# Performance work log

Measured on AMD Instinct MI355X. Metric: run time of the kernel, lower is better.

## Reference

```python
import jax, jax.numpy as jnp
import numpy as np

NH, HD, MBS = 32, 64, 16   # num_heads, head_dim, mini_batch_size
BASE_LR = 1.0
ROPE_BASE = 10000.0
EPS = 1e-6


def _rotate_half(x):
    x1, x2 = jnp.split(x, 2, axis=-1)
    return jnp.concatenate((-x2, x1), axis=-1)


def _permute_qk(x):
    B, H, L, D = x.shape
    return x.reshape(B, H, L, D // 2, 2).swapaxes(-1, -2).reshape(B, H, L, D)


def _undo_permute_qk(x):
    B, H, L, D = x.shape
    return x.reshape(B, H, L, 2, D // 2).swapaxes(-1, -2).reshape(B, H, L, D)


def _ln_fwd(x, gamma, beta):
    mu = x.mean(-1, keepdims=True)
    var = x.var(-1, keepdims=True)
    return gamma * ((x - mu) / jnp.sqrt(var + EPS)) + beta


def _ln_fused_l2_bwd(x, target, gamma, beta):
    # grad of 0.5*||LN(x) - target||^2 wrt x, fused
    D = x.shape[-1]
    mu = x.mean(-1, keepdims=True)
    std = jnp.sqrt(x.var(-1, keepdims=True) + EPS)
    x_hat = (x - mu) / std
    y = gamma * x_hat + beta
    g = (y - target) * gamma
    return (D * g - g.sum(-1, keepdims=True) - x_hat * (g * x_hat).sum(-1, keepdims=True)) / (D * std)


def setup_inputs() -> dict:
    key = jax.random.key(0)
    ks = jax.random.split(key, 8)
    B, L, C, OUT = 4, 2048, 2048, 768
    s = 0.02
    return {
        "hidden_states": jax.random.normal(ks[0], (B, L, C), jnp.float32),
        "position_ids": jnp.broadcast_to(jnp.arange(L, dtype=jnp.int32)[None], (B, L)),
        "Wq": jax.random.normal(ks[1], (C, C), jnp.float32) * s,
        "Wk": jax.random.normal(ks[2], (C, C), jnp.float32) * s,
        "Wv": jax.random.normal(ks[3], (C, C), jnp.float32) * s,
        "Wo": jax.random.normal(ks[4], (C, OUT), jnp.float32) * s,
        "W1": jax.random.normal(ks[5], (NH, HD, HD), jnp.float32) * s,
        "b1": jnp.zeros((NH, 1, HD), jnp.float32),
        "ttt_lr_weight": jax.random.normal(ks[6], (NH, 1, C), jnp.float32) * s,
        "ttt_lr_bias": jnp.zeros((NH, 1), jnp.float32),
        "learnable_token_idx": jnp.zeros((MBS,), jnp.float32),
        "ttt_norm_weight": jnp.ones((NH, HD), jnp.float32),
        "ttt_norm_bias": jnp.zeros((NH, HD), jnp.float32),
        "post_norm_weight": jnp.ones((C,), jnp.float32),
        "post_norm_bias": jnp.zeros((C,), jnp.float32),
    }


def reference(hidden_states, position_ids, Wq, Wk, Wv, Wo, W1, b1,
              ttt_lr_weight, ttt_lr_bias, learnable_token_idx,
              ttt_norm_weight, ttt_norm_bias, post_norm_weight, post_norm_bias):
    B, L, C = hidden_states.shape
    NM = L // MBS
    # QKV projections -> [B, NH, L, HD]
    XQ = (hidden_states @ Wq).reshape(B, L, NH, HD).transpose(0, 2, 1, 3)
    XK = (hidden_states @ Wk).reshape(B, L, NH, HD).transpose(0, 2, 1, 3)
    XV = (hidden_states @ Wv).reshape(B, L, NH, HD).transpose(0, 2, 1, 3)
    # RoPE on positions modulo the mini-batch size
    pos = (position_ids % MBS).astype(jnp.float32)  # [B, L]
    inv_freq = 1.0 / (ROPE_BASE ** (jnp.arange(0, HD, 2, dtype=jnp.float32) / HD))
    freqs = pos[..., None] * inv_freq               # [B, L, HD/2]
    emb = jnp.concatenate((freqs, freqs), axis=-1)  # [B, L, HD]
    cos = jnp.cos(emb)[:, None]                     # [B, 1, L, HD]
    sin = jnp.sin(emb)[:, None]
    XQ, XK = _permute_qk(XQ), _permute_qk(XK)
    XQ = XQ * cos + _rotate_half(XQ) * sin
    XK = XK * cos + _rotate_half(XK) * sin
    XQ, XK = _undo_permute_qk(XQ), _undo_permute_qk(XK)
    # reshape into mini-batches: [B, NH, NM, K, HD]
    X = hidden_states.reshape(B, NM, MBS, C)
    XQ = XQ.reshape(B, NH, NM, MBS, HD)
    XK = XK.reshape(B, NH, NM, MBS, HD)
    XV = XV.reshape(B, NH, NM, MBS, HD)
    # eta: per-token learnable LR gate
    ttt_lr = jax.nn.sigmoid(
        jnp.einsum('bnkc,hdc->bhnkd', X, ttt_lr_weight)
        + ttt_lr_bias.reshape(1, NH, 1, 1, 1))              # [B,NH,NM,K,1]
    ttt_lr_eta = BASE_LR * ttt_lr.transpose(0, 1, 2, 4, 3) / HD  # [B,NH,NM,1,K]
    token_idx = jnp.clip(1.0 / jnp.arange(1, MBS + 1, dtype=jnp.float32)
                         + learnable_token_idx, 0.0, None)
    token_eta = token_idx.reshape(1, 1, 1, MBS, 1)
    eta = token_eta * ttt_lr_eta                            # [B,NH,NM,K,K]
    # TTT-Linear dual-form mini-batch scan
    ln_w = ttt_norm_weight.reshape(1, NH, 1, HD)
    ln_b = ttt_norm_bias.reshape(1, NH, 1, HD)
    W1_0 = jnp.broadcast_to(W1[None], (B, NH, HD, HD))
    b1_0 = jnp.broadcast_to(b1[None], (B, NH, 1, HD))
    tril = jnp.tril(jnp.ones((MBS, MBS), hidden_states.dtype))

    def step(carry, xs):
        W1_s, b1_s = carry
        xq, xk, xv, eta_m = xs                 # [B,NH,K,HD], eta_m [B,NH,K,K]
        Z1 = xk @ W1_s + b1_s
        target = xv - xk
        grad = _ln_fused_l2_bwd(Z1, target, ln_w, ln_b)
        Attn = tril * (xq @ xk.swapaxes(-1, -2))
        b1_bar = b1_s - (tril * eta_m) @ grad
        Z1_bar = xq @ W1_s - (eta_m * Attn) @ grad + b1_bar
        last_eta = eta_m[:, :, -1, :, None]    # [B,NH,K,1]
        W1_new = W1_s - (last_eta * xk).swapaxes(-1, -2) @ grad
        b1_new = b1_s - jnp.sum(last_eta * grad, axis=-2, keepdims=True)
        out = xq + _ln_fwd(Z1_bar, ln_w, ln_b)
        return (W1_new, b1_new), out

    xs = (XQ.transpose(2, 0, 1, 3, 4), XK.transpose(2, 0, 1, 3, 4),
          XV.transpose(2, 0, 1, 3, 4), eta.transpose(2, 0, 1, 3, 4))
    _, outs = jax.lax.scan(step, (W1_0, b1_0), xs)   # [NM,B,NH,K,HD]
    out = outs.transpose(1, 2, 0, 3, 4).reshape(B, NH, L, HD)
    out = out.transpose(0, 2, 1, 3).reshape(B, L, C)
    # post LayerNorm (eps 1e-6) and output projection
    mu = out.mean(-1, keepdims=True)
    var = out.var(-1, keepdims=True)
    out = (out - mu) / jnp.sqrt(var + EPS) * post_norm_weight + post_norm_bias
    return out @ Wo
```

## Files before the change

kernel.cpp:

```cpp
#include <hip/hip_runtime.h>
#include <cstddef>
#include <cstdint>

#define B_DIM   4
#define L_SEQ   2048
#define C_DIM   2048
#define OUT_DIM 768
#define NHEADS  32
#define HDIM    64
#define MBS_    16
#define NMINI   128
#define EPS_    1e-6f

typedef _Float16 half8 __attribute__((ext_vector_type(8)));
typedef float floatx4 __attribute__((ext_vector_type(4)));

__device__ __forceinline__ void glds16(const void* g, void* l) {
    __builtin_amdgcn_global_load_lds(
        (const __attribute__((address_space(1))) uint32_t*)g,
        (__attribute__((address_space(3))) uint32_t*)l, 16, 0, 0);
}

__device__ __forceinline__ void split8(const float4 a, const float4 b,
                                       half8& hi, half8& lo) {
    const float x[8] = {a.x, a.y, a.z, a.w, b.x, b.y, b.z, b.w};
#pragma unroll
    for (int e = 0; e < 8; e++) {
        const _Float16 h = (_Float16)x[e];
        hi[e] = h;
        lo[e] = (_Float16)(x[e] - (float)h);
    }
}

#define MFMA3(ACC, AH, AL, BH, BL)                                             \
    ACC = __builtin_amdgcn_mfma_f32_16x16x32_f16((AH), (BH), ACC, 0, 0, 0);    \
    ACC = __builtin_amdgcn_mfma_f32_16x16x32_f16((AH), (BL), ACC, 0, 0, 0);    \
    ACC = __builtin_amdgcn_mfma_f32_16x16x32_f16((AL), (BH), ACC, 0, 0, 0);

#define BARRIER_LGKM() __asm volatile("s_waitcnt lgkmcnt(0)\n\ts_barrier" ::: "memory")
#define WAIT_VM0()     __asm volatile("s_waitcnt vmcnt(0)" ::: "memory")

__global__ __launch_bounds__(256)
void gemm_af32(const float* __restrict__ A,
               const _Float16* __restrict__ Bhi, const _Float16* __restrict__ Blo,
               float* __restrict__ Cout, int mode, int doRope)
{
    __shared__ __align__(16) float    sA[4096];
    __shared__ __align__(16) _Float16 sBhi[4096];
    __shared__ __align__(16) _Float16 sBlo[4096];
    const int tid = threadIdx.x;
    const int m0 = blockIdx.y * 128, n0 = blockIdx.x * 128;
    const int K = 2048;

    size_t gA[4]; float* lA[4];
#pragma unroll
    for (int I = 0; I < 4; I++) {
        const int c = I * 256 + tid;
        const int row = c >> 3, seg = (c & 7) ^ (row & 7);
        gA[I] = (size_t)(m0 + row) * K + seg * 4;
        lA[I] = &sA[c * 4];
    }
    size_t gB[2]; _Float16 *lBh[2], *lBl[2];
#pragma unroll
    for (int I = 0; I < 2; I++) {
        const int c = I * 256 + tid;
        const int row = c >> 2, seg = (c & 3) ^ ((row >> 1) & 3);
        gB[I] = (size_t)(n0 + row) * K + seg * 8;
        lBh[I] = &sBhi[c * 8];
        lBl[I] = &sBlo[c * 8];
    }

    const int lane = tid & 63, quad = lane >> 4, lc = lane & 15;
    const int wv = tid >> 6, wm = wv & 1, wn = wv >> 1;
    int offA0[4], offA1[4], offB[4];
#pragma unroll
    for (int i = 0; i < 4; i++) {
        const int rA = wm * 64 + i * 16 + lc;
        offA0[i] = (rA * 8 + ((2 * quad)     ^ (rA & 7))) * 4;
        offA1[i] = (rA * 8 + ((2 * quad + 1) ^ (rA & 7))) * 4;
    }
#pragma unroll
    for (int j = 0; j < 4; j++) {
        const int rB = wn * 64 + j * 16 + lc;
        offB[j] = (rB * 4 + (quad ^ ((rB >> 1) & 3))) * 8;
    }

    floatx4 acc[4][4];
#pragma unroll
    for (int i = 0; i < 4; i++)
#pragma unroll
        for (int j = 0; j < 4; j++) acc[i][j] = (floatx4)0.0f;

    for (int k0 = 0; k0 < K; k0 += 32) {
        __syncthreads();
#pragma unroll
        for (int I = 0; I < 4; I++) glds16(A + gA[I] + k0, lA[I]);
#pragma unroll
        for (int I = 0; I < 2; I++) {
            glds16(Bhi + gB[I] + k0, lBh[I]);
            glds16(Blo + gB[I] + k0, lBl[I]);
        }
        __syncthreads();

        half8 ah[4], al[4], bh[4], bl[4];
#pragma unroll
        for (int i = 0; i < 4; i++) {
            const float4 va = *(const float4*)&sA[offA0[i]];
            const float4 vb = *(const float4*)&sA[offA1[i]];
            split8(va, vb, ah[i], al[i]);
        }
#pragma unroll
        for (int j = 0; j < 4; j++) {
            bh[j] = *(const half8*)&sBhi[offB[j]];
            bl[j] = *(const half8*)&sBlo[offB[j]];
        }
#pragma unroll
        for (int i = 0; i < 4; i++)
#pragma unroll
            for (int j = 0; j < 4; j++) {
                MFMA3(acc[i][j], ah[i], al[i], bh[j], bl[j]);
            }
    }

    float cs[4][4], sn[4][4];
    if (doRope) {
#pragma unroll
        for (int j = 0; j < 4; j++) {
            const int ii = ((j * 16 + lc) & 63) >> 1;
            const float invf = expf(-(float)ii * 0.28782313662425574f);
#pragma unroll
            for (int r = 0; r < 4; r++) {
                const float ang = (float)(quad * 4 + r) * invf;
                sincosf(ang, &sn[j][r], &cs[j][r]);
            }
        }
    }
    const int oddcol = lc & 1;
#pragma unroll
    for (int i = 0; i < 4; i++) {
#pragma unroll
        for (int j = 0; j < 4; j++) {
            floatx4 v = acc[i][j];
            if (doRope) {
#pragma unroll
                for (int r = 0; r < 4; r++) {
                    const float partner = __shfl_xor(v[r], 1);
                    v[r] = v[r] * cs[j][r] + partner * (oddcol ? sn[j][r] : -sn[j][r]);
                }
            }
            const int n = n0 + wn * 64 + j * 16 + lc;
            if (mode == 0) {
                const int h = (n >> 6) & 31, d = n & 63;
#pragma unroll
                for (int r = 0; r < 4; r++) {
                    const int m = m0 + wm * 64 + i * 16 + quad * 4 + r;
                    const int b = m >> 11, li = m & 2047;
                    Cout[((size_t)(b * 32 + h) * 2048 + li) * 64 + d] = v[r];
                }
            } else {
#pragma unroll
                for (int r = 0; r < 4; r++) {
                    const int m = m0 + wm * 64 + i * 16 + quad * 4 + r;
                    Cout[(size_t)m * OUT_DIM + n] = v[r];
                }
            }
        }
    }
}

__global__ __launch_bounds__(256)
void wtrans_kernel(const float* __restrict__ W, _Float16* __restrict__ BThi,
                   _Float16* __restrict__ BTlo, int Nw)
{
    __shared__ float tile[32][33];
    const int t = threadIdx.x, tx = t & 31, ty = t >> 5;
    const int n0 = blockIdx.x * 32, k0 = blockIdx.y * 32;
    const int K = 2048;
#pragma unroll
    for (int r = 0; r < 4; r++)
        tile[ty + r * 8][tx] = W[(size_t)(k0 + ty + r * 8) * Nw + n0 + tx];
    __syncthreads();
#pragma unroll
    for (int r = 0; r < 4; r++) {
        const float val = tile[tx][ty + r * 8];
        const _Float16 hh = (_Float16)val;
        const size_t o = (size_t)(n0 + ty + r * 8) * K + k0 + tx;
        BThi[o] = hh;
        BTlo[o] = (_Float16)(val - (float)hh);
    }
}

__global__ __launch_bounds__(256)
void lr_kernel(const float* __restrict__ hidden, const float* __restrict__ wlr,
               const float* __restrict__ lr_bias, float* __restrict__ lrs)
{
    __shared__ float sRow[2048];
    __shared__ float sPart[32][9];
    const int m = blockIdx.x;
    const int t = threadIdx.x;
    const float* row = hidden + (size_t)m * C_DIM;
#pragma unroll
    for (int j = 0; j < 8; j++) sRow[t + j * 256] = row[t + j * 256];
    __syncthreads();
    const int h = t >> 3, p = t & 7;
    const float* w = wlr + (size_t)h * C_DIM;
    float s = 0.0f;
#pragma unroll 8
    for (int k = 0; k < 64; k++) {
        const int c = k * 32 + p * 4;
        const float4 a = *(const float4*)(sRow + c);
        const float4 b = *(const float4*)(w + c);
        s += a.x * b.x + a.y * b.y + a.z * b.z + a.w * b.w;
    }
    sPart[h][p] = s;
    __syncthreads();
    if (t < 32) {
        float v = 0.0f;
#pragma unroll
        for (int p2 = 0; p2 < 8; p2++) v += sPart[t][p2];
        v += lr_bias[t];
        const float sig = 1.0f / (1.0f + expf(-v));
        lrs[((size_t)(m >> 11) * NHEADS + t) * L_SEQ + (m & 2047)] = sig;
    }
}

__global__ __launch_bounds__(256, 1)
void scan_v6(const float* __restrict__ XQ, const float* __restrict__ XK,
             float* __restrict__ XVo, const float* __restrict__ LRS,
             const float* __restrict__ W1i, const float* __restrict__ b1i,
             const float* __restrict__ lt, const float* __restrict__ lnw,
             const float* __restrict__ lnb)
{
    __shared__ __align__(16) float sXq[2][1024];
    __shared__ __align__(16) float sXk[2][1024];
    __shared__ __align__(16) float sXv[2][1024];
    __shared__ __align__(16) float sW1T[4096];
    __shared__ __align__(16) float sGt[64 * 36];
    __shared__ __align__(16) float sKt[64 * 36];
    __shared__ __align__(16) float sCf[16 * 36];
    __shared__ __align__(16) float sRedA[16 * 8];
    __shared__ __align__(16) float sRedB[16 * 8];
    __shared__ __align__(16) float sRedC[16 * 8];
    __shared__ __align__(16) float sB1[64];
    __shared__ __align__(16) float sEta[32];

    const int t = threadIdx.x;
    const int lane = t & 63, q = lane >> 4, lc = lane & 15;
    const int w = t >> 6;
    const int col = 16 * w + lc;
    const int bh = blockIdx.x, h = bh & 31;

    int srcOffW;
    {
        const int c = w * 64 + lane;
        const int row = c >> 4, seg = (c & 15) ^ (row & 15);
        srcOffW = row * 64 + seg * 4;
    }

    float tokR[4];
#pragma unroll
    for (int r = 0; r < 4; r++)
        tokR[r] = fmaxf(1.0f / (float)(4 * q + r + 1) + lt[4 * q + r], 0.0f);
    const float tok15 = fmaxf(1.0f / 16.0f + lt[15], 0.0f);
    const float gamC = lnw[h * 64 + col], betC = lnb[h * 64 + col];

    if (t < 64) sB1[t] = b1i[h * 64 + t];
    if (t < 32) sEta[t] = 0.0f;
    for (int z = t; z < 1024; z += 256) {
        const int r = z >> 4, c = 16 + (z & 15);
        sGt[r * 36 + c] = 0.0f;
        sKt[r * 36 + c] = 0.0f;
    }
    { const int r = t >> 4, c = 16 + (t & 15); sCf[r * 36 + c] = 0.0f; }

    float w1s[4][4];
#pragma unroll
    for (int t4 = 0; t4 < 4; t4++)
#pragma unroll
        for (int r = 0; r < 4; r++)
            w1s[t4][r] = W1i[h * 4096 + (16 * t4 + lc) * 64 + (16 * w + 4 * q + r)];
#pragma unroll
    for (int t4 = 0; t4 < 4; t4++)
#pragma unroll
        for (int r = 0; r < 4; r++) {
            const int nn = 16 * w + 4 * q + r, k = 16 * t4 + lc;
            sW1T[nn * 64 + ((((k >> 2) ^ (nn & 15)) << 2) | (k & 3))] = w1s[t4][r];
        }

    const size_t base = (size_t)bh * L_SEQ * HDIM;
    const float* xq_g = XQ + base;
    const float* xk_g = XK + base;
    float* xv_g = XVo + base;
    const float* lr_g = LRS + (size_t)bh * L_SEQ;

    glds16(xq_g + srcOffW, &sXq[0][w * 256]);
    glds16(xk_g + srcOffW, &sXk[0][w * 256]);
    glds16(xv_g + srcOffW, &sXv[0][w * 256]);
    float clr = lr_g[lc];

    for (int n = 0; n < NMINI; n++) {
        const int buf = n & 1, nb = buf ^ 1;
        WAIT_VM0();
        BARRIER_LGKM();

        const float etaC = clr * (1.0f / 64.0f);
        if (w == 0 && t < 16) sEta[t] = etaC;
        const int np = (n + 1) & (NMINI - 1);
        const size_t go = (size_t)np * 1024;
        glds16(xq_g + go + srcOffW, &sXq[nb][w * 256]);
        glds16(xk_g + go + srcOffW, &sXk[nb][w * 256]);
        glds16(xv_g + go + srcOffW, &sXv[nb][w * 256]);
        const float nlr = lr_g[np * 16 + lc];

        const float b1c = sB1[col];

        {
            const int phys = q + 4 * w;
            const float4 v = *(const float4*)&sXk[buf][lc * 64 + phys * 4];
            const int cb = 4 * (phys ^ lc);
            const float leC = tok15 * etaC;
            sKt[(cb + 0) * 36 + lc] = v.x * leC;
            sKt[(cb + 1) * 36 + lc] = v.y * leC;
            sKt[(cb + 2) * 36 + lc] = v.z * leC;
            sKt[(cb + 3) * 36 + lc] = v.w * leC;
        }

        half8 qh[2], ql[2], kh[2], kl[2], wh[2], wl[2];
#pragma unroll
        for (int f = 0; f < 2; f++) {
            const int ca = (8 * f + 2 * q) ^ lc, cb2 = (8 * f + 2 * q + 1) ^ lc;
            {
                const float4 u0 = *(const float4*)&sXq[buf][lc * 64 + ca * 4];
                const float4 u1 = *(const float4*)&sXq[buf][lc * 64 + cb2 * 4];
                split8(u0, u1, qh[f], ql[f]);
            }
            {
                const float4 u0 = *(const float4*)&sXk[buf][lc * 64 + ca * 4];
                const float4 u1 = *(const float4*)&sXk[buf][lc * 64 + cb2 * 4];
                split8(u0, u1, kh[f], kl[f]);
            }
            {
                const int rw = 16 * w + lc;
                const float4 u0 = *(const float4*)&sW1T[rw * 64 + ca * 4];
                const float4 u1 = *(const float4*)&sW1T[rw * 64 + cb2 * 4];
                split8(u0, u1, wh[f], wl[f]);
            }
        }

        floatx4 at = (floatx4)0.0f, z1a = (floatx4)0.0f, zba = (floatx4)0.0f;
        if (w == 0) {
#pragma unroll
            for (int f = 0; f < 2; f++) { MFMA3(at, qh[f], ql[f], kh[f], kl[f]); }
        }
#pragma unroll
        for (int f = 0; f < 2; f++) {
            MFMA3(z1a, kh[f], kl[f], wh[f], wl[f]);
            MFMA3(zba, qh[f], ql[f], wh[f], wl[f]);
        }

        float z[4], s1[4], s2[4];
#pragma unroll
        for (int r = 0; r < 4; r++) { z[r] = z1a[r] + b1c; s1[r] = z[r]; s2[r] = z[r] * z[r]; }
#pragma unroll
        for (int o = 1; o < 16; o <<= 1)
#pragma unroll
            for (int r = 0; r < 4; r++) { s1[r] += __shfl_xor(s1[r], o); s2[r] += __shfl_xor(s2[r], o); }
        if (lc == 0)
#pragma unroll
            for (int r = 0; r < 4; r++) {
                sRedA[(4 * q + r) * 8 + w] = s1[r];
                sRedA[(4 * q + r) * 8 + 4 + w] = s2[r];
            }
        BARRIER_LGKM();
        float mu[4], rs[4];
#pragma unroll
        for (int r = 0; r < 4; r++) {
            const float4 a = *(const float4*)&sRedA[(4 * q + r) * 8];
            const float4 b = *(const float4*)&sRedA[(4 * q + r) * 8 + 4];
            const float m1 = (a.x + a.y + a.z + a.w) * (1.0f / 64.0f);
            mu[r] = m1;
            rs[r] = rsqrtf((b.x + b.y + b.z + b.w) * (1.0f / 64.0f) - m1 * m1 + EPS_);
        }

        float gg[4], xh[4], g1[4], g2[4];
#pragma unroll
        for (int r = 0; r < 4; r++) {
            const int row = 4 * q + r;
            const int ad = row * 64 + (((((col >> 2) ^ row) & 15) << 2) | (col & 3));
            xh[r] = (z[r] - mu[r]) * rs[r];
            const float tgt = sXv[buf][ad] - sXk[buf][ad];
            gg[r] = (gamC * xh[r] + betC - tgt) * gamC;
            g1[r] = gg[r];
            g2[r] = gg[r] * xh[r];
        }
#pragma unroll
        for (int o = 1; o < 16; o <<= 1)
#pragma unroll
            for (int r = 0; r < 4; r++) { g1[r] += __shfl_xor(g1[r], o); g2[r] += __shfl_xor(g2[r], o); }
        if (lc == 0)
#pragma unroll
            for (int r = 0; r < 4; r++) {
                sRedB[(4 * q + r) * 8 + w] = g1[r];
                sRedB[(4 * q + r) * 8 + 4 + w] = g2[r];
            }
        BARRIER_LGKM();
        {
            float4 g4;
#pragma unroll
            for (int r = 0; r < 4; r++) {
                const float4 a = *(const float4*)&sRedB[(4 * q + r) * 8];
                const float4 b = *(const float4*)&sRedB[(4 * q + r) * 8 + 4];
                const float G1 = a.x + a.y + a.z + a.w;
                const float G2 = b.x + b.y + b.z + b.w;
                ((float*)&g4)[r] = (64.0f * gg[r] - G1 - xh[r] * G2) * rs[r] * (1.0f / 64.0f);
            }
            *(float4*)&sGt[col * 36 + 4 * q] = g4;
        }
        if (w == 0) {
#pragma unroll
            for (int r = 0; r < 4; r++) {
                const int i = 4 * q + r;
                sCf[i * 36 + lc] = (lc <= i) ? -tokR[r] * etaC * (at[r] + 1.0f) : 0.0f;
            }
        }
        BARRIER_LGKM();

        half8 cfh, cfl, gth, gtl;
        {
            const float4 u0 = *(const float4*)&sCf[lc * 36 + 8 * q];
            const float4 u1 = *(const float4*)&sCf[lc * 36 + 8 * q + 4];
            split8(u0, u1, cfh, cfl);
        }
        {
            const int rw = 16 * w + lc;
            const float4 u0 = *(const float4*)&sGt[rw * 36 + 8 * q];
            const float4 u1 = *(const float4*)&sGt[rw * 36 + 8 * q + 4];
            split8(u0, u1, gth, gtl);
        }
        MFMA3(zba, cfh, cfl, gth, gtl);
#pragma unroll
        for (int t4 = 0; t4 < 4; t4++) {
            half8 kth, ktl;
            const float4 u0 = *(const float4*)&sKt[(16 * t4 + lc) * 36 + 8 * q];
            const float4 u1 = *(const float4*)&sKt[(16 * t4 + lc) * 36 + 8 * q + 4];
            split8(u0, u1, kth, ktl);
            floatx4 up = (floatx4)0.0f;
            MFMA3(up, gth, gtl, kth, ktl);
#pragma unroll
            for (int r = 0; r < 4; r++) w1s[t4][r] -= up[r];
        }

        float z2[4];
#pragma unroll
        for (int r = 0; r < 4; r++) { z2[r] = zba[r] + b1c; s1[r] = z2[r]; s2[r] = z2[r] * z2[r]; }
#pragma unroll
        for (int o = 1; o < 16; o <<= 1)
#pragma unroll
            for (int r = 0; r < 4; r++) { s1[r] += __shfl_xor(s1[r], o); s2[r] += __shfl_xor(s2[r], o); }
        if (lc == 0)
#pragma unroll
            for (int r = 0; r < 4; r++) {
                sRedC[(4 * q + r) * 8 + w] = s1[r];
                sRedC[(4 * q + r) * 8 + 4 + w] = s2[r];
            }
        BARRIER_LGKM();
#pragma unroll
        for (int r = 0; r < 4; r++) {
            const float4 a = *(const float4*)&sRedC[(4 * q + r) * 8];
            const float4 b = *(const float4*)&sRedC[(4 * q + r) * 8 + 4];
            const float m1 = (a.x + a.y + a.z + a.w) * (1.0f / 64.0f);
            mu[r] = m1;
            rs[r] = rsqrtf((b.x + b.y + b.z + b.w) * (1.0f / 64.0f) - m1 * m1 + EPS_);
        }
#pragma unroll
        for (int r = 0; r < 4; r++) {
            const int row = 4 * q + r;
            const int ad = row * 64 + (((((col >> 2) ^ row) & 15) << 2) | (col & 3));
            xv_g[n * 1024 + row * 64 + col] =
                sXq[buf][ad] + gamC * ((z2[r] - mu[r]) * rs[r]) + betC;
        }

        {
            const float4 e0 = *(const float4*)&sEta[8 * q];
            const float4 e1 = *(const float4*)&sEta[8 * q + 4];
            const float ev[8] = {e0.x, e0.y, e0.z, e0.w, e1.x, e1.y, e1.z, e1.w};
            float p = 0.0f;
#pragma unroll
            for (int jj = 0; jj < 8; jj++)
                p += ((float)gth[jj] + (float)gtl[jj]) * ev[jj];
            p += __shfl_xor(p, 16);
            if (q == 0) sB1[col] -= tok15 * p;
        }

#pragma unroll
        for (int t4 = 0; t4 < 4; t4++)
#pragma unroll
            for (int r = 0; r < 4; r++) {
                const int nn = 16 * w + 4 * q + r, k = 16 * t4 + lc;
                sW1T[nn * 64 + ((((k >> 2) ^ (nn & 15)) << 2) | (k & 3))] = w1s[t4][r];
            }
        clr = nlr;
    }
}

__global__ __launch_bounds__(256)
void postln_kernel(const float* __restrict__ Ob, const float* __restrict__ pnw,
                   const float* __restrict__ pnb, float* __restrict__ XN)
{
    const int m = blockIdx.x;
    const int b = m >> 11, l = m & 2047;
    const int t = threadIdx.x;
    float v[8];
    float s1 = 0.0f, s2 = 0.0f;
    const float* bas = Ob + (size_t)b * NHEADS * L_SEQ * HDIM + (size_t)l * HDIM;
#pragma unroll
    for (int j = 0; j < 8; j++) {
        const int c = t + j * 256;
        const int hh = c >> 6, d = c & 63;
        const float x = bas[(size_t)hh * (L_SEQ * HDIM) + d];
        v[j] = x; s1 += x; s2 += x * x;
    }
#pragma unroll
    for (int o = 1; o < 64; o <<= 1) { s1 += __shfl_xor(s1, o); s2 += __shfl_xor(s2, o); }
    __shared__ float r1[4], r2[4];
    const int w = t >> 6;
    if ((t & 63) == 0) { r1[w] = s1; r2[w] = s2; }
    __syncthreads();
    s1 = r1[0] + r1[1] + r1[2] + r1[3];
    s2 = r2[0] + r2[1] + r2[2] + r2[3];
    const float mu = s1 * (1.0f / 2048.0f);
    const float var = s2 * (1.0f / 2048.0f) - mu * mu;
    const float rstd = rsqrtf(var + EPS_);
    float* o = XN + (size_t)m * C_DIM;
#pragma unroll
    for (int j = 0; j < 8; j++) {
        const int c = t + j * 256;
        o[c] = (v[j] - mu) * rstd * pnw[c] + pnb[c];
    }
}

extern "C" void kernel_launch(void* const* d_in, const int* in_sizes, int n_in,
                              void* d_out, int out_size, void* d_ws, size_t ws_size,
                              hipStream_t stream)
{
    (void)in_sizes; (void)n_in; (void)out_size; (void)ws_size;
    const float* hidden  = (const float*)d_in[0];
    const float* Wq      = (const float*)d_in[2];
    const float* Wk      = (const float*)d_in[3];
    const float* Wv      = (const float*)d_in[4];
    const float* Wo      = (const float*)d_in[5];
    const float* W1      = (const float*)d_in[6];
    const float* b1      = (const float*)d_in[7];
    const float* wlr     = (const float*)d_in[8];
    const float* lr_bias = (const float*)d_in[9];
    const float* lt      = (const float*)d_in[10];
    const float* lnw     = (const float*)d_in[11];
    const float* lnb     = (const float*)d_in[12];
    const float* pnw     = (const float*)d_in[13];
    const float* pnb     = (const float*)d_in[14];

    const size_t TEN = (size_t)B_DIM * NHEADS * L_SEQ * HDIM;
    float* XQ  = (float*)d_ws;
    float* XK  = XQ + TEN;
    float* XVo = XK + TEN;
    float* LRS = XVo + TEN;
    const dim3 blk(256);

    _Float16* BThi = (_Float16*)d_out;
    _Float16* BTlo = BThi + (size_t)C_DIM * C_DIM;

    lr_kernel<<<dim3(B_DIM * L_SEQ), blk, 0, stream>>>(hidden, wlr, lr_bias, LRS);

    const float* Wmats[3] = {Wq, Wk, Wv};
    float* outs[3] = {XQ, XK, XVo};
    for (int p = 0; p < 3; p++) {
        wtrans_kernel<<<dim3(64, 64), blk, 0, stream>>>(Wmats[p], BThi, BTlo, C_DIM);
        gemm_af32<<<dim3(16, 64), blk, 0, stream>>>(hidden, BThi, BTlo,
                                                    outs[p], 0, (p < 2) ? 1 : 0);
    }
    scan_v6<<<dim3(B_DIM * NHEADS), blk, 0, stream>>>(XQ, XK, XVo, LRS,
                                                      W1, b1, lt, lnw, lnb);
    float* XN = XQ;
    _Float16* WThi = (_Float16*)XK;
    _Float16* WTlo = WThi + (size_t)OUT_DIM * C_DIM;
    postln_kernel<<<dim3(B_DIM * L_SEQ), blk, 0, stream>>>(XVo, pnw, pnb, XN);
    wtrans_kernel<<<dim3(24, 64), blk, 0, stream>>>(Wo, WThi, WTlo, OUT_DIM);
    gemm_af32<<<dim3(6, 64), blk, 0, stream>>>(XN, WThi, WTlo,
                                               (float*)d_out, 1, 0);
}
```

Before: 1.611 ms.

## Restructure TTT scan to cut barriers and pass gradients via shuffles

Result: faster. 1.512 ms (-6.1%).

```diff
diff --git a/kernel.cpp b/kernel.cpp
--- a/kernel.cpp
+++ b/kernel.cpp
@@ -32,13 +32,19 @@
     }
 }
 
+__device__ __forceinline__ void split8f(const float x[8], half8& hi, half8& lo) {
+#pragma unroll
+    for (int e = 0; e < 8; e++) {
+        const _Float16 h = (_Float16)x[e];
+        hi[e] = h;
+        lo[e] = (_Float16)(x[e] - (float)h);
+    }
+}
+
 #define MFMA3(ACC, AH, AL, BH, BL)                                             \
     ACC = __builtin_amdgcn_mfma_f32_16x16x32_f16((AH), (BH), ACC, 0, 0, 0);    \
     ACC = __builtin_amdgcn_mfma_f32_16x16x32_f16((AH), (BL), ACC, 0, 0, 0);    \
     ACC = __builtin_amdgcn_mfma_f32_16x16x32_f16((AL), (BH), ACC, 0, 0, 0);
-
-#define BARRIER_LGKM() __asm volatile("s_waitcnt lgkmcnt(0)\n\ts_barrier" ::: "memory")
-#define WAIT_VM0()     __asm volatile("s_waitcnt vmcnt(0)" ::: "memory")
 
 __global__ __launch_bounds__(256)
 void gemm_af32(const float* __restrict__ A,
@@ -225,7 +231,7 @@
 }
 
 __global__ __launch_bounds__(256, 1)
-void scan_v6(const float* __restrict__ XQ, const float* __restrict__ XK,
+void scan_v8(const float* __restrict__ XQ, const float* __restrict__ XK,
              float* __restrict__ XVo, const float* __restrict__ LRS,
              const float* __restrict__ W1i, const float* __restrict__ b1i,
              const float* __restrict__ lt, const float* __restrict__ lnw,
@@ -235,14 +241,12 @@
     __shared__ __align__(16) float sXk[2][1024];
     __shared__ __align__(16) float sXv[2][1024];
     __shared__ __align__(16) float sW1T[4096];
-    __shared__ __align__(16) float sGt[64 * 36];
     __shared__ __align__(16) float sKt[64 * 36];
     __shared__ __align__(16) float sCf[16 * 36];
-    __shared__ __align__(16) float sRedA[16 * 8];
-    __shared__ __align__(16) float sRedB[16 * 8];
-    __shared__ __align__(16) float sRedC[16 * 8];
+    __shared__ __align__(16) float sRedA[128];
+    __shared__ __align__(16) float sRedB[128];
+    __shared__ __align__(16) float sRedC[128];
     __shared__ __align__(16) float sB1[64];
-    __shared__ __align__(16) float sEta[32];
 
     const int t = threadIdx.x;
     const int lane = t & 63, q = lane >> 4, lc = lane & 15;
@@ -250,11 +254,12 @@
     const int col = 16 * w + lc;
     const int bh = blockIdx.x, h = bh & 31;
 
-    int srcOffW;
+    int srcOffW, ldsOff;
     {
         const int c = w * 64 + lane;
         const int row = c >> 4, seg = (c & 15) ^ (row & 15);
         srcOffW = row * 64 + seg * 4;
+        ldsOff = c * 4;
     }
 
     float tokR[4];
@@ -265,10 +270,8 @@
     const float gamC = lnw[h * 64 + col], betC = lnb[h * 64 + col];
 
     if (t < 64) sB1[t] = b1i[h * 64 + t];
-    if (t < 32) sEta[t] = 0.0f;
     for (int z = t; z < 1024; z += 256) {
         const int r = z >> 4, c = 16 + (z & 15);
-        sGt[r * 36 + c] = 0.0f;
         sKt[r * 36 + c] = 0.0f;
     }
     { const int r = t >> 4, c = 16 + (t & 15); sCf[r * 36 + c] = 0.0f; }
@@ -293,26 +296,44 @@
     float* xv_g = XVo + base;
     const float* lr_g = LRS + (size_t)bh * L_SEQ;
 
-    glds16(xq_g + srcOffW, &sXq[0][w * 256]);
-    glds16(xk_g + srcOffW, &sXk[0][w * 256]);
-    glds16(xv_g + srcOffW, &sXv[0][w * 256]);
+    {
+        const float4 q0 = *(const float4*)(xq_g + srcOffW);
+        const float4 k0 = *(const float4*)(xk_g + srcOffW);
+        const float4 v0 = *(const float4*)(xv_g + srcOffW);
+        *(float4*)&sXq[0][ldsOff] = q0;
+        *(float4*)&sXk[0][ldsOff] = k0;
+        *(float4*)&sXv[0][ldsOff] = v0;
+    }
     float clr = lr_g[lc];
+    __syncthreads();
+
+    int adR[4];
+#pragma unroll
+    for (int r = 0; r < 4; r++) {
+        const int row = 4 * q + r;
+        adR[r] = row * 64 + (((((col >> 2) ^ row) & 15) << 2) | (col & 3));
+    }
 
     for (int n = 0; n < NMINI; n++) {
         const int buf = n & 1, nb = buf ^ 1;
-        WAIT_VM0();
-        BARRIER_LGKM();
-
-        const float etaC = clr * (1.0f / 64.0f);
-        if (w == 0 && t < 16) sEta[t] = etaC;
+
         const int np = (n + 1) & (NMINI - 1);
         const size_t go = (size_t)np * 1024;
-        glds16(xq_g + go + srcOffW, &sXq[nb][w * 256]);
-        glds16(xk_g + go + srcOffW, &sXk[nb][w * 256]);
-        glds16(xv_g + go + srcOffW, &sXv[nb][w * 256]);
+        const float4 nq = *(const float4*)(xq_g + go + srcOffW);
+        const float4 nk = *(const float4*)(xk_g + go + srcOffW);
+        const float4 nv = *(const float4*)(xv_g + go + srcOffW);
         const float nlr = lr_g[np * 16 + lc];
 
+        const float etaC = clr * (1.0f / 64.0f);
         const float b1c = sB1[col];
+
+        float xvR[4], xkR[4], xqR[4];
+#pragma unroll
+        for (int r = 0; r < 4; r++) {
+            xvR[r] = sXv[buf][adR[r]];
+            xkR[r] = sXk[buf][adR[r]];
+            xqR[r] = sXq[buf][adR[r]];
+        }
 
         {
             const int phys = q + 4 * w;
@@ -358,6 +379,14 @@
             MFMA3(zba, qh[f], ql[f], wh[f], wl[f]);
         }
 
+        if (w == 0) {
+#pragma unroll
+            for (int r = 0; r < 4; r++) {
+                const int i = 4 * q + r;
+                sCf[i * 36 + lc] = (lc <= i) ? -tokR[r] * etaC * (at[r] + 1.0f) : 0.0f;
+            }
+        }
+
         float z[4], s1[4], s2[4];
 #pragma unroll
         for (int r = 0; r < 4; r++) { z[r] = z1a[r] + b1c; s1[r] = z[r]; s2[r] = z[r] * z[r]; }
@@ -371,7 +400,8 @@
                 sRedA[(4 * q + r) * 8 + w] = s1[r];
                 sRedA[(4 * q + r) * 8 + 4 + w] = s2[r];
             }
-        BARRIER_LGKM();
+        __syncthreads();
+
         float mu[4], rs[4];
 #pragma unroll
         for (int r = 0; r < 4; r++) {
@@ -385,10 +415,8 @@
         float gg[4], xh[4], g1[4], g2[4];
 #pragma unroll
         for (int r = 0; r < 4; r++) {
-            const int row = 4 * q + r;
-            const int ad = row * 64 + (((((col >> 2) ^ row) & 15) << 2) | (col & 3));
             xh[r] = (z[r] - mu[r]) * rs[r];
-            const float tgt = sXv[buf][ad] - sXk[buf][ad];
+            const float tgt = xvR[r] - xkR[r];
             gg[r] = (gamC * xh[r] + betC - tgt) * gamC;
             g1[r] = gg[r];
             g2[r] = gg[r] * xh[r];
@@ -403,41 +431,34 @@
                 sRedB[(4 * q + r) * 8 + w] = g1[r];
                 sRedB[(4 * q + r) * 8 + 4 + w] = g2[r];
             }
-        BARRIER_LGKM();
+        __syncthreads();
+
+        float gradReg[4];
+#pragma unroll
+        for (int r = 0; r < 4; r++) {
+            const float4 a = *(const float4*)&sRedB[(4 * q + r) * 8];
+            const float4 b = *(const float4*)&sRedB[(4 * q + r) * 8 + 4];
+            const float G1 = a.x + a.y + a.z + a.w;
+            const float G2 = b.x + b.y + b.z + b.w;
+            gradReg[r] = (64.0f * gg[r] - G1 - xh[r] * G2) * rs[r] * (1.0f / 64.0f);
+        }
+        half8 gth, gtl;
         {
-            float4 g4;
-#pragma unroll
-            for (int r = 0; r < 4; r++) {
-                const float4 a = *(const float4*)&sRedB[(4 * q + r) * 8];
-                const float4 b = *(const float4*)&sRedB[(4 * q + r) * 8 + 4];
-                const float G1 = a.x + a.y + a.z + a.w;
-                const float G2 = b.x + b.y + b.z + b.w;
-                ((float*)&g4)[r] = (64.0f * gg[r] - G1 - xh[r] * G2) * rs[r] * (1.0f / 64.0f);
-            }
-            *(float4*)&sGt[col * 36 + 4 * q] = g4;
-        }
-        if (w == 0) {
-#pragma unroll
-            for (int r = 0; r < 4; r++) {
-                const int i = 4 * q + r;
-                sCf[i * 36 + lc] = (lc <= i) ? -tokR[r] * etaC * (at[r] + 1.0f) : 0.0f;
-            }
-        }
-        BARRIER_LGKM();
-
-        half8 cfh, cfl, gth, gtl;
+            float gv[8];
+#pragma unroll
+            for (int jj = 0; jj < 8; jj++) {
+                const float v = __shfl(gradReg[jj & 3], ((q * 8 + jj) >> 2) * 16 + lc);
+                gv[jj] = (q < 2) ? v : 0.0f;
+            }
+            split8f(gv, gth, gtl);
+        }
         {
+            half8 cfh, cfl;
             const float4 u0 = *(const float4*)&sCf[lc * 36 + 8 * q];
             const float4 u1 = *(const float4*)&sCf[lc * 36 + 8 * q + 4];
             split8(u0, u1, cfh, cfl);
-        }
-        {
-            const int rw = 16 * w + lc;
-            const float4 u0 = *(const float4*)&sGt[rw * 36 + 8 * q];
-            const float4 u1 = *(const float4*)&sGt[rw * 36 + 8 * q + 4];
-            split8(u0, u1, gth, gtl);
-        }
-        MFMA3(zba, cfh, cfl, gth, gtl);
+            MFMA3(zba, cfh, cfl, gth, gtl);
+        }
 #pragma unroll
         for (int t4 = 0; t4 < 4; t4++) {
             half8 kth, ktl;
@@ -449,7 +470,25 @@
 #pragma unroll
             for (int r = 0; r < 4; r++) w1s[t4][r] -= up[r];
         }
-
+        {
+            float p = 0.0f;
+#pragma unroll
+            for (int r = 0; r < 4; r++)
+                p += __shfl(etaC, 4 * q + r) * gradReg[r];
+            p += __shfl_xor(p, 16);
+            p += __shfl_xor(p, 32);
+            if (q == 0) sB1[col] -= tok15 * p;
+        }
+        *(float4*)&sXq[nb][ldsOff] = nq;
+        *(float4*)&sXk[nb][ldsOff] = nk;
+        *(float4*)&sXv[nb][ldsOff] = nv;
+#pragma unroll
+        for (int t4 = 0; t4 < 4; t4++)
+#pragma unroll
+            for (int r = 0; r < 4; r++) {
+                const int nn = 16 * w + 4 * q + r, k = 16 * t4 + lc;
+                sW1T[nn * 64 + ((((k >> 2) ^ (nn & 15)) << 2) | (k & 3))] = w1s[t4][r];
+            }
         float z2[4];
 #pragma unroll
         for (int r = 0; r < 4; r++) { z2[r] = zba[r] + b1c; s1[r] = z2[r]; s2[r] = z2[r] * z2[r]; }
@@ -463,42 +502,18 @@
                 sRedC[(4 * q + r) * 8 + w] = s1[r];
                 sRedC[(4 * q + r) * 8 + 4 + w] = s2[r];
             }
-        BARRIER_LGKM();
+        __syncthreads();
+
 #pragma unroll
         for (int r = 0; r < 4; r++) {
             const float4 a = *(const float4*)&sRedC[(4 * q + r) * 8];
             const float4 b = *(const float4*)&sRedC[(4 * q + r) * 8 + 4];
             const float m1 = (a.x + a.y + a.z + a.w) * (1.0f / 64.0f);
-            mu[r] = m1;
-            rs[r] = rsqrtf((b.x + b.y + b.z + b.w) * (1.0f / 64.0f) - m1 * m1 + EPS_);
-        }
-#pragma unroll
-        for (int r = 0; r < 4; r++) {
+            const float rr = rsqrtf((b.x + b.y + b.z + b.w) * (1.0f / 64.0f) - m1 * m1 + EPS_);
             const int row = 4 * q + r;
-            const int ad = row * 64 + (((((col >> 2) ^ row) & 15) << 2) | (col & 3));
             xv_g[n * 1024 + row * 64 + col] =
-                sXq[buf][ad] + gamC * ((z2[r] - mu[r]) * rs[r]) + betC;
-        }
-
-        {
-            const float4 e0 = *(const float4*)&sEta[8 * q];
-            const float4 e1 = *(const float4*)&sEta[8 * q + 4];
-            const float ev[8] = {e0.x, e0.y, e0.z, e0.w, e1.x, e1.y, e1.z, e1.w};
-            float p = 0.0f;
-#pragma unroll
-            for (int jj = 0; jj < 8; jj++)
-                p += ((float)gth[jj] + (float)gtl[jj]) * ev[jj];
-            p += __shfl_xor(p, 16);
-            if (q == 0) sB1[col] -= tok15 * p;
-        }
-
-#pragma unroll
-        for (int t4 = 0; t4 < 4; t4++)
-#pragma unroll
-            for (int r = 0; r < 4; r++) {
-                const int nn = 16 * w + 4 * q + r, k = 16 * t4 + lc;
-                sW1T[nn * 64 + ((((k >> 2) ^ (nn & 15)) << 2) | (k & 3))] = w1s[t4][r];
-            }
+                xqR[r] + gamC * ((z2[r] - m1) * rr) + betC;
+        }
         clr = nlr;
     }
 }
@@ -578,7 +593,7 @@
         gemm_af32<<<dim3(16, 64), blk, 0, stream>>>(hidden, BThi, BTlo,
                                                     outs[p], 0, (p < 2) ? 1 : 0);
     }
-    scan_v6<<<dim3(B_DIM * NHEADS), blk, 0, stream>>>(XQ, XK, XVo, LRS,
+    scan_v8<<<dim3(B_DIM * NHEADS), blk, 0, stream>>>(XQ, XK, XVo, LRS,
                                                       W1, b1, lt, lnw, lnb);
     float* XN = XQ;
     _Float16* WThi = (_Float16*)XK;
```
